# Optimization experiments

Hardware: AMD Instinct MI355X
Metric: run time of the kernel (lower is better)

The kernel has to match this reference:

```python
import jax, jax.numpy as jnp
import numpy as np

TAU = 1.0            # temperature (self.temperature.item())
FAST_WEIGHT_DECAY = 0.01
FAST_WEIGHT_LR = 0.01

B, IN, H = 128, 1024, 1024


def setup_inputs() -> dict:
    key = jax.random.key(0)
    k = jax.random.split(key, 6)
    scale_ih = 1.0 / np.sqrt(IN)
    scale_hh = np.sqrt(2.0 / (H + H))  # xavier_uniform-like std
    return {
        "x_t": jax.random.normal(k[0], (B, IN), jnp.float32),
        "h_prev": jax.random.normal(k[1], (B, H), jnp.float32),
        "W_ih": jax.random.normal(k[2], (H, IN), jnp.float32) * scale_ih,
        "b_ih": jnp.zeros((H,), jnp.float32),
        "W_hh_fixed": jax.random.normal(k[3], (H, H), jnp.float32) * scale_hh,
        "W_hh_virtual": jnp.zeros((H, H), jnp.float32),
        "gumbel_u": jax.random.uniform(k[4], (B, H, H), jnp.float32),
    }


def reference(x_t, h_prev, W_ih, b_ih, W_hh_fixed, W_hh_virtual, gumbel_u):
    # input contribution: Linear(input_size, hidden_size)
    input_contrib = x_t @ W_ih.T + b_ih                      # (B, H)

    # logits scaled by temperature once, then gumbel_softmax divides by tau again
    logits = (W_hh_fixed + W_hh_virtual) / TAU               # (H, H)
    eps = 1e-9
    g = -jnp.log(-jnp.log(jnp.clip(gumbel_u, eps, 1.0 - eps)))  # Gumbel(0,1), (B,H,H)
    y = jax.nn.softmax((logits[None, :, :] + g) / TAU, axis=2)  # soft sampling, (B,H,H)

    # weighted exchange: each output neuron o reduces sampled weights against h_prev
    contrib = jnp.einsum('boh,bh->bo', y, h_prev)            # (B, H)
    h_next = jnp.tanh(input_contrib + contrib)               # (B, H)

    # Hebbian fast-weight update (no_grad in original)
    hebbian = jnp.einsum('bo,bh->oh', h_next, h_prev) / B    # mean over batch, (H,H)
    W_hh_virtual_new = jax.lax.stop_gradient(
        W_hh_virtual * (1.0 - FAST_WEIGHT_DECAY) + hebbian * FAST_WEIGHT_LR
    )
    return h_next, W_hh_virtual_new
```

## Files before the change

### kernel.cpp

```cpp
#include <hip/hip_runtime.h>
#include <hip/hip_bf16.h>
#include <cstddef>

#define B_DIM  128
#define IN_DIM 1024
#define H_DIM  1024

constexpr float kDecay   = 1.0f - 0.01f;
constexpr float kLrOverB = 0.01f / 128.0f;

typedef float f32x4 __attribute__((ext_vector_type(4)));

__global__ __launch_bounds__(256) void exp_logits(
    const float* __restrict__ W_f,
    const float* __restrict__ W_v,
    float* __restrict__ E)
{
    const int i = blockIdx.x * 256 + threadIdx.x;
    const float4 a = reinterpret_cast<const float4*>(W_f)[i];
    const float4 b = reinterpret_cast<const float4*>(W_v)[i];
    float4 e;
    e.x = __expf(a.x + b.x); e.y = __expf(a.y + b.y);
    e.z = __expf(a.z + b.z); e.w = __expf(a.w + b.w);
    reinterpret_cast<float4*>(E)[i] = e;
}

__global__ __launch_bounds__(256) void input_gemm(
    const float* __restrict__ x_t,
    const float* __restrict__ W_ih,
    const float* __restrict__ b_ih,
    float* __restrict__ ic)
{
    const int o0 = blockIdx.x * 64;
    const int b0 = blockIdx.y * 16;
    const int t  = threadIdx.x;

    __shared__ float Wt[64][68];
    __shared__ float xs[64][17];

    const int tx = t & 15;
    const int ty = t >> 4;

    float acc[4] = {0.f, 0.f, 0.f, 0.f};

    for (int kc = 0; kc < IN_DIM / 64; ++kc) {
        const int k0 = kc * 64;

#pragma unroll
        for (int ii = 0; ii < 4; ++ii) {
            const int i  = t + 256 * ii;
            const int r  = i >> 4;
            const int c4 = (i & 15) * 4;
            const float4 wv = *reinterpret_cast<const float4*>(
                &W_ih[(size_t)(o0 + r) * IN_DIM + k0 + c4]);
            Wt[c4 + 0][r] = wv.x; Wt[c4 + 1][r] = wv.y;
            Wt[c4 + 2][r] = wv.z; Wt[c4 + 3][r] = wv.w;
        }
        {
            const int br = t >> 4;
            const int c4 = (t & 15) * 4;
            const float4 xv = *reinterpret_cast<const float4*>(
                &x_t[(size_t)(b0 + br) * IN_DIM + k0 + c4]);
            xs[c4 + 0][br] = xv.x; xs[c4 + 1][br] = xv.y;
            xs[c4 + 2][br] = xv.z; xs[c4 + 3][br] = xv.w;
        }
        __syncthreads();

#pragma unroll 8
        for (int k = 0; k < 64; ++k) {
            const float  xb = xs[k][ty];
            const float4 wv = *reinterpret_cast<const float4*>(&Wt[k][4 * tx]);
            acc[0] = fmaf(wv.x, xb, acc[0]);
            acc[1] = fmaf(wv.y, xb, acc[1]);
            acc[2] = fmaf(wv.z, xb, acc[2]);
            acc[3] = fmaf(wv.w, xb, acc[3]);
        }
        __syncthreads();
    }

    const int o = o0 + 4 * tx;
    const int b = b0 + ty;
    float4 r;
    r.x = acc[0] + b_ih[o + 0];
    r.y = acc[1] + b_ih[o + 1];
    r.z = acc[2] + b_ih[o + 2];
    r.w = acc[3] + b_ih[o + 3];
    *reinterpret_cast<float4*>(&ic[(size_t)b * H_DIM + o]) = r;
}

__global__ __launch_bounds__(256, 4) void fused_rows(
    const float* __restrict__ h_prev,
    const float* __restrict__ E,
    const float* __restrict__ gu,
    const float* __restrict__ ic,
    float* __restrict__ h_next)
{
    const int b0 = blockIdx.x * 4;
    const int o0 = blockIdx.y * 8;
    const int t  = threadIdx.x;
    const int w  = t >> 6, lane = t & 63;

    __shared__ __align__(16) float e_s[8 * H_DIM];

    {
        const float4* src = reinterpret_cast<const float4*>(E) + (size_t)o0 * 256;
        float4*       dst = reinterpret_cast<float4*>(e_s);
#pragma unroll
        for (int ii = 0; ii < 8; ++ii) dst[t + 256 * ii] = src[t + 256 * ii];
    }
    __syncthreads();

    const int b = b0 + w;

    const float4* hp4 = reinterpret_cast<const float4*>(h_prev + (size_t)b * H_DIM);
    float4 p[4];
#pragma unroll
    for (int j = 0; j < 4; ++j) p[j] = hp4[lane + 64 * j];

    const f32x4*  g4 = reinterpret_cast<const f32x4*>(gu)
                     + ((size_t)b * H_DIM + o0) * 256;
    const float4* e4 = reinterpret_cast<const float4*>(e_s);

    f32x4 ua[4], ub[4];
    float s[8], d[8];

#pragma unroll
    for (int j = 0; j < 4; ++j)
        ua[j] = __builtin_nontemporal_load(g4 + lane + 64 * j);

#pragma unroll
    for (int oi = 0; oi < 8; ++oi) {
        if (oi < 7) {
            const f32x4* gn = g4 + (size_t)(oi + 1) * 256;
            if ((oi & 1) == 0) {
#pragma unroll
                for (int j = 0; j < 4; ++j)
                    ub[j] = __builtin_nontemporal_load(gn + lane + 64 * j);
            } else {
#pragma unroll
                for (int j = 0; j < 4; ++j)
                    ua[j] = __builtin_nontemporal_load(gn + lane + 64 * j);
            }
        }

        float sum = 0.f, dot = 0.f;
#pragma unroll
        for (int j = 0; j < 4; ++j) {
            const f32x4  uu = (oi & 1) ? ub[j] : ua[j];
            const float4 ee = e4[oi * 256 + lane + 64 * j];
            const float4 pp = p[j];
            const float q0 = __fdividef(ee.x, -__log2f(fmaxf(uu.x, 1e-9f)));
            const float q1 = __fdividef(ee.y, -__log2f(fmaxf(uu.y, 1e-9f)));
            const float q2 = __fdividef(ee.z, -__log2f(fmaxf(uu.z, 1e-9f)));
            const float q3 = __fdividef(ee.w, -__log2f(fmaxf(uu.w, 1e-9f)));
            sum += (q0 + q1) + (q2 + q3);
            dot = fmaf(q0, pp.x, dot);
            dot = fmaf(q1, pp.y, dot);
            dot = fmaf(q2, pp.z, dot);
            dot = fmaf(q3, pp.w, dot);
        }
        s[oi] = sum;
        d[oi] = dot;
    }

#pragma unroll
    for (int off = 32; off > 0; off >>= 1) {
#pragma unroll
        for (int r = 0; r < 8; ++r) {
            s[r] += __shfl_xor(s[r], off, 64);
            d[r] += __shfl_xor(d[r], off, 64);
        }
    }

    if (lane == 0) {
        const size_t base = (size_t)b * H_DIM + o0;
        const float4 i0 = *reinterpret_cast<const float4*>(ic + base);
        const float4 i1 = *reinterpret_cast<const float4*>(ic + base + 4);
        float4 r0, r1;
        r0.x = tanhf(i0.x + __fdividef(d[0], s[0]));
        r0.y = tanhf(i0.y + __fdividef(d[1], s[1]));
        r0.z = tanhf(i0.z + __fdividef(d[2], s[2]));
        r0.w = tanhf(i0.w + __fdividef(d[3], s[3]));
        r1.x = tanhf(i1.x + __fdividef(d[4], s[4]));
        r1.y = tanhf(i1.y + __fdividef(d[5], s[5]));
        r1.z = tanhf(i1.z + __fdividef(d[6], s[6]));
        r1.w = tanhf(i1.w + __fdividef(d[7], s[7]));
        *reinterpret_cast<float4*>(h_next + base)     = r0;
        *reinterpret_cast<float4*>(h_next + base + 4) = r1;
    }
}

__global__ __launch_bounds__(256) void hebbian_update(
    const float* __restrict__ h_next,
    const float* __restrict__ h_prev,
    const float* __restrict__ W_v,
    float* __restrict__ W_out)
{
    const int h0 = blockIdx.x * 64;
    const int o0 = blockIdx.y * 64;
    const int t  = threadIdx.x;

    __shared__ __align__(16) float hn_s[B_DIM][64];
    __shared__ __align__(16) float hp_s[B_DIM][64];

#pragma unroll
    for (int i = 0; i < 32; ++i) {
        const int e  = t + 256 * i;
        const int bb = e >> 6;
        const int cc = e & 63;
        hn_s[bb][cc] = h_next[(size_t)bb * H_DIM + o0 + cc];
        hp_s[bb][cc] = h_prev[(size_t)bb * H_DIM + h0 + cc];
    }
    __syncthreads();

    const int tx = t & 15;
    const int ty = t >> 4;

    float acc[4][4] = {{0.f}};

#pragma unroll 8
    for (int b = 0; b < B_DIM; ++b) {
        const float4 av = reinterpret_cast<const float4*>(hn_s[b])[ty];
        const float4 bv = reinterpret_cast<const float4*>(hp_s[b])[tx];
        const float aa[4] = {av.x, av.y, av.z, av.w};
        const float bb[4] = {bv.x, bv.y, bv.z, bv.w};
#pragma unroll
        for (int a = 0; a < 4; ++a)
#pragma unroll
            for (int c = 0; c < 4; ++c)
                acc[a][c] = fmaf(aa[a], bb[c], acc[a][c]);
    }

#pragma unroll
    for (int a = 0; a < 4; ++a) {
        const int o = o0 + 4 * ty + a;
        const size_t base = (size_t)o * H_DIM + h0 + 4 * tx;
        const float4 wv = *reinterpret_cast<const float4*>(W_v + base);
        float4 r;
        r.x = wv.x * kDecay + acc[a][0] * kLrOverB;
        r.y = wv.y * kDecay + acc[a][1] * kLrOverB;
        r.z = wv.z * kDecay + acc[a][2] * kLrOverB;
        r.w = wv.w * kDecay + acc[a][3] * kLrOverB;
        *reinterpret_cast<float4*>(W_out + base) = r;
    }
}

extern "C" void kernel_launch(void* const* d_in, const int* in_sizes, int n_in,
                              void* d_out, int out_size, void* d_ws, size_t ws_size,
                              hipStream_t stream)
{
    const float* x_t    = (const float*)d_in[0];
    const float* h_prev = (const float*)d_in[1];
    const float* W_ih   = (const float*)d_in[2];
    const float* b_ih   = (const float*)d_in[3];
    const float* W_f    = (const float*)d_in[4];
    const float* W_v    = (const float*)d_in[5];
    const float* gu     = (const float*)d_in[6];

    float* out    = (float*)d_out;
    float* h_next = out;
    float* W_out  = out + (size_t)B_DIM * H_DIM;

    float* E  = (float*)d_ws;
    float* ic = E + (size_t)H_DIM * H_DIM;

    exp_logits<<<dim3(H_DIM * H_DIM / 1024), 256, 0, stream>>>(W_f, W_v, E);

    input_gemm<<<dim3(H_DIM / 64, B_DIM / 16), 256, 0, stream>>>(
        x_t, W_ih, b_ih, ic);

    fused_rows<<<dim3(B_DIM / 4, H_DIM / 8), 256, 0, stream>>>(
        h_prev, E, gu, ic, h_next);

    hebbian_update<<<dim3(H_DIM / 64, H_DIM / 64), 256, 0, stream>>>(
        h_next, h_prev, W_v, W_out);
}
```

Before: 144.1 us.

## Drop LDS staging of exp logits and double-buffer global loads two rows ahead

Removes the shared-memory copy of the 8 exp-logit rows and the block barrier. Each wave now reads E directly from global memory (L2-resident, shared across blocks) alongside the gumbel stream. Prefetching moves from one row ahead to two rows ahead, using two register buffers for both streams. This removes LDS traffic and the barrier and puts more loads in flight. The cost is higher register pressure and more global/L2 requests for E, since each wave re-reads E instead of sharing it through LDS.

```diff
diff --git a/kernel.cpp b/kernel.cpp
--- a/kernel.cpp
+++ b/kernel.cpp
@@ -99,55 +99,41 @@
     const int o0 = blockIdx.y * 8;
     const int t  = threadIdx.x;
     const int w  = t >> 6, lane = t & 63;
-
-    __shared__ __align__(16) float e_s[8 * H_DIM];
-
-    {
-        const float4* src = reinterpret_cast<const float4*>(E) + (size_t)o0 * 256;
-        float4*       dst = reinterpret_cast<float4*>(e_s);
-#pragma unroll
-        for (int ii = 0; ii < 8; ++ii) dst[t + 256 * ii] = src[t + 256 * ii];
-    }
-    __syncthreads();
-
-    const int b = b0 + w;
+    const int b  = b0 + w;
 
     const float4* hp4 = reinterpret_cast<const float4*>(h_prev + (size_t)b * H_DIM);
     float4 p[4];
 #pragma unroll
     for (int j = 0; j < 4; ++j) p[j] = hp4[lane + 64 * j];
 
-    const f32x4*  g4 = reinterpret_cast<const f32x4*>(gu)
-                     + ((size_t)b * H_DIM + o0) * 256;
-    const float4* e4 = reinterpret_cast<const float4*>(e_s);
-
-    f32x4 ua[4], ub[4];
+    const f32x4* g4 = reinterpret_cast<const f32x4*>(gu)
+                    + ((size_t)b * H_DIM + o0) * 256;
+    const f32x4* e4 = reinterpret_cast<const f32x4*>(E) + (size_t)o0 * 256;
+
+    f32x4 ug[2][4];
+    f32x4 ue[2][4];
     float s[8], d[8];
 
 #pragma unroll
-    for (int j = 0; j < 4; ++j)
-        ua[j] = __builtin_nontemporal_load(g4 + lane + 64 * j);
+    for (int j = 0; j < 4; ++j) {
+        ug[0][j] = __builtin_nontemporal_load(g4 + lane + 64 * j);
+        ue[0][j] = e4[lane + 64 * j];
+    }
+#pragma unroll
+    for (int j = 0; j < 4; ++j) {
+        ug[1][j] = __builtin_nontemporal_load(g4 + 256 + lane + 64 * j);
+        ue[1][j] = e4[256 + lane + 64 * j];
+    }
 
 #pragma unroll
     for (int oi = 0; oi < 8; ++oi) {
-        if (oi < 7) {
-            const f32x4* gn = g4 + (size_t)(oi + 1) * 256;
-            if ((oi & 1) == 0) {
-#pragma unroll
-                for (int j = 0; j < 4; ++j)
-                    ub[j] = __builtin_nontemporal_load(gn + lane + 64 * j);
-            } else {
-#pragma unroll
-                for (int j = 0; j < 4; ++j)
-                    ua[j] = __builtin_nontemporal_load(gn + lane + 64 * j);
-            }
-        }
+        const int cur = oi & 1;
 
         float sum = 0.f, dot = 0.f;
 #pragma unroll
         for (int j = 0; j < 4; ++j) {
-            const f32x4  uu = (oi & 1) ? ub[j] : ua[j];
-            const float4 ee = e4[oi * 256 + lane + 64 * j];
+            const f32x4 uu = ug[cur][j];
+            const f32x4 ee = ue[cur][j];
             const float4 pp = p[j];
             const float q0 = __fdividef(ee.x, -__log2f(fmaxf(uu.x, 1e-9f)));
             const float q1 = __fdividef(ee.y, -__log2f(fmaxf(uu.y, 1e-9f)));
@@ -161,6 +147,16 @@
         }
         s[oi] = sum;
         d[oi] = dot;
+
+        if (oi < 6) {
+            const f32x4* gn = g4 + (size_t)(oi + 2) * 256;
+            const f32x4* en = e4 + (size_t)(oi + 2) * 256;
+#pragma unroll
+            for (int j = 0; j < 4; ++j) {
+                ug[cur][j] = __builtin_nontemporal_load(gn + lane + 64 * j);
+                ue[cur][j] = en[lane + 64 * j];
+            }
+        }
     }
 
 #pragma unroll
```

New measurement: 147.9 us (median of 2 runs). +2.6%, slower.

## Fuse exp-logits into fused_rows and deepen gumbel prefetch to four rows

Applied to the files above, without the earlier changes.

Removes the separate exp_logits kernel: each fused_rows block now reads W_fixed and W_virtual for its 8 rows and computes exp into shared memory itself, dropping one launch and the E workspace write/read. The gumbel prefetch is deepened from double-buffering (one row ahead) to four rows in flight, with launch bounds lowered from 4 to 3 blocks per SM to give room for the extra registers. The cost is redundant exp work, since every one of the 32 batch-blocks recomputes the same rows, plus possibly lower occupancy.

```diff
diff --git a/kernel.cpp b/kernel.cpp
--- a/kernel.cpp
+++ b/kernel.cpp
@@ -10,20 +10,6 @@
 constexpr float kLrOverB = 0.01f / 128.0f;
 
 typedef float f32x4 __attribute__((ext_vector_type(4)));
-
-__global__ __launch_bounds__(256) void exp_logits(
-    const float* __restrict__ W_f,
-    const float* __restrict__ W_v,
-    float* __restrict__ E)
-{
-    const int i = blockIdx.x * 256 + threadIdx.x;
-    const float4 a = reinterpret_cast<const float4*>(W_f)[i];
-    const float4 b = reinterpret_cast<const float4*>(W_v)[i];
-    float4 e;
-    e.x = __expf(a.x + b.x); e.y = __expf(a.y + b.y);
-    e.z = __expf(a.z + b.z); e.w = __expf(a.w + b.w);
-    reinterpret_cast<float4*>(E)[i] = e;
-}
 
 __global__ __launch_bounds__(256) void input_gemm(
     const float* __restrict__ x_t,
@@ -88,9 +74,10 @@
     *reinterpret_cast<float4*>(&ic[(size_t)b * H_DIM + o]) = r;
 }
 
-__global__ __launch_bounds__(256, 4) void fused_rows(
+__global__ __launch_bounds__(256, 3) void fused_rows(
     const float* __restrict__ h_prev,
-    const float* __restrict__ E,
+    const float* __restrict__ W_f,
+    const float* __restrict__ W_v,
     const float* __restrict__ gu,
     const float* __restrict__ ic,
     float* __restrict__ h_next)
@@ -103,10 +90,18 @@
     __shared__ __align__(16) float e_s[8 * H_DIM];
 
     {
-        const float4* src = reinterpret_cast<const float4*>(E) + (size_t)o0 * 256;
+        const float4* f4 = reinterpret_cast<const float4*>(W_f) + (size_t)o0 * 256;
+        const float4* v4 = reinterpret_cast<const float4*>(W_v) + (size_t)o0 * 256;
         float4*       dst = reinterpret_cast<float4*>(e_s);
 #pragma unroll
-        for (int ii = 0; ii < 8; ++ii) dst[t + 256 * ii] = src[t + 256 * ii];
+        for (int ii = 0; ii < 8; ++ii) {
+            const float4 a = f4[t + 256 * ii];
+            const float4 b = v4[t + 256 * ii];
+            float4 ee;
+            ee.x = __expf(a.x + b.x); ee.y = __expf(a.y + b.y);
+            ee.z = __expf(a.z + b.z); ee.w = __expf(a.w + b.w);
+            dst[t + 256 * ii] = ee;
+        }
     }
     __syncthreads();
 
@@ -121,32 +116,23 @@
                      + ((size_t)b * H_DIM + o0) * 256;
     const float4* e4 = reinterpret_cast<const float4*>(e_s);
 
-    f32x4 ua[4], ub[4];
+    f32x4 ug[4][4];
     float s[8], d[8];
 
 #pragma unroll
-    for (int j = 0; j < 4; ++j)
-        ua[j] = __builtin_nontemporal_load(g4 + lane + 64 * j);
+    for (int tp = 0; tp < 4; ++tp)
+#pragma unroll
+        for (int j = 0; j < 4; ++j)
+            ug[tp][j] = __builtin_nontemporal_load(g4 + tp * 256 + lane + 64 * j);
 
 #pragma unroll
     for (int oi = 0; oi < 8; ++oi) {
-        if (oi < 7) {
-            const f32x4* gn = g4 + (size_t)(oi + 1) * 256;
-            if ((oi & 1) == 0) {
-#pragma unroll
-                for (int j = 0; j < 4; ++j)
-                    ub[j] = __builtin_nontemporal_load(gn + lane + 64 * j);
-            } else {
-#pragma unroll
-                for (int j = 0; j < 4; ++j)
-                    ua[j] = __builtin_nontemporal_load(gn + lane + 64 * j);
-            }
-        }
+        const int sl = oi & 3;
 
         float sum = 0.f, dot = 0.f;
 #pragma unroll
         for (int j = 0; j < 4; ++j) {
-            const f32x4  uu = (oi & 1) ? ub[j] : ua[j];
+            const f32x4  uu = ug[sl][j];
             const float4 ee = e4[oi * 256 + lane + 64 * j];
             const float4 pp = p[j];
             const float q0 = __fdividef(ee.x, -__log2f(fmaxf(uu.x, 1e-9f)));
@@ -161,6 +147,13 @@
         }
         s[oi] = sum;
         d[oi] = dot;
+
+        if (oi < 4) {
+            const f32x4* gn = g4 + (size_t)(oi + 4) * 256;
+#pragma unroll
+            for (int j = 0; j < 4; ++j)
+                ug[sl][j] = __builtin_nontemporal_load(gn + lane + 64 * j);
+        }
     }
 
 #pragma unroll
@@ -261,16 +254,13 @@
     float* h_next = out;
     float* W_out  = out + (size_t)B_DIM * H_DIM;
 
-    float* E  = (float*)d_ws;
-    float* ic = E + (size_t)H_DIM * H_DIM;
-
-    exp_logits<<<dim3(H_DIM * H_DIM / 1024), 256, 0, stream>>>(W_f, W_v, E);
+    float* ic = (float*)d_ws;
 
     input_gemm<<<dim3(H_DIM / 64, B_DIM / 16), 256, 0, stream>>>(
         x_t, W_ih, b_ih, ic);
 
     fused_rows<<<dim3(B_DIM / 4, H_DIM / 8), 256, 0, stream>>>(
-        h_prev, E, gu, ic, h_next);
+        h_prev, W_f, W_v, gu, ic, h_next);
 
     hebbian_update<<<dim3(H_DIM / 64, H_DIM / 64), 256, 0, stream>>>(
         h_next, h_prev, W_v, W_out);
```

Measured after the change: 145.5 us. About the same (+1.0%).
